# Performance work log

Measured on AMD Instinct MI355X. Metric: run time of the kernel, lower is better.

Reference implementation:

```python
import jax, jax.numpy as jnp
import numpy as np

EPS = 1e-5

def _ln(x, g, b):
    m = jnp.mean(x, axis=-1, keepdims=True)
    v = jnp.mean((x - m) ** 2, axis=-1, keepdims=True)
    return (x - m) * jax.lax.rsqrt(v + EPS) * g + b


def setup_inputs() -> dict:
    key = jax.random.key(0)
    B, T, C, H, A = 4, 1024, 1024, 16, 64
    ks = jax.random.split(key, 16)
    s = 0.02
    inp = {
        "x": jax.random.normal(ks[0], (B, T, C), jnp.float32),
        "ln1_g": jnp.ones((C,), jnp.float32), "ln1_b": jnp.zeros((C,), jnp.float32),
        "ln2_g": jnp.ones((C,), jnp.float32), "ln2_b": jnp.zeros((C,), jnp.float32),
        "ln3_g": jnp.ones((C,), jnp.float32), "ln3_b": jnp.zeros((C,), jnp.float32),
        "wq": jax.random.normal(ks[1], (C, C), jnp.float32) * s, "bq": jnp.zeros((C,), jnp.float32),
        "wk": jax.random.normal(ks[2], (C, C), jnp.float32) * s, "bk": jnp.zeros((C,), jnp.float32),
        "wv": jax.random.normal(ks[3], (C, C), jnp.float32) * s, "bv": jnp.zeros((C,), jnp.float32),
        "wo": jax.random.normal(ks[4], (C, C), jnp.float32) * s, "bo": jnp.zeros((C,), jnp.float32),
        "w1": jax.random.normal(ks[5], (C, 4 * C), jnp.float32) * s, "b1": jnp.zeros((4 * C,), jnp.float32),
        "w2": jax.random.normal(ks[6], (4 * C, C), jnp.float32) * s, "b2": jnp.zeros((C,), jnp.float32),
        "wd": jax.random.normal(ks[7], (C, A), jnp.float32) * 1e-4, "bd": jnp.zeros((A,), jnp.float32),
        "wu": jax.random.normal(ks[8], (A, C), jnp.float32) * 1e-4, "bu": jnp.zeros((C,), jnp.float32),
    }
    return inp


def _block(x, ln1_g, ln1_b, ln2_g, ln2_b, ln3_g, ln3_b,
           wq, bq, wk, bk, wv, bv, wo, bo, w1, b1, w2, b2, wd, bd, wu, bu):
    B, T, C = x.shape
    H = 16
    D = C // H
    normed = _ln(x, ln3_g, ln3_b)  # ln3 of original input, used by adapter

    # --- causal self-attention on ln1(x) ---
    h = _ln(x, ln1_g, ln1_b)
    q = (h @ wq + bq).reshape(B, T, H, D)
    k = (h @ wk + bk).reshape(B, T, H, D)
    v = (h @ wv + bv).reshape(B, T, H, D)
    att = jnp.einsum('bqhd,bkhd->bhqk', q, k) * (1.0 / np.sqrt(D))
    causal = jnp.tril(jnp.ones((T, T), bool))
    att = jnp.where(causal, att, -jnp.inf)
    att = jax.nn.softmax(att, axis=-1)
    y = jnp.einsum('bhqk,bkhd->bqhd', att, v).reshape(B, T, C)
    attn_out = y @ wo + bo

    hidden = x + attn_out
    # --- MLP on ln2(hidden) ---
    m = _ln(hidden, ln2_g, ln2_b)
    mlp_out = jax.nn.gelu(m @ w1 + b1, approximate=False) @ w2 + b2
    forward_states = hidden + mlp_out

    # --- adapter on ln3(original x) ---
    a = jax.nn.relu(normed @ wd + bd) @ wu + bu

    # dropout is identity (p=0 / eval)
    return hidden + forward_states + a


def reference(x, ln1_g, ln1_b, ln2_g, ln2_b, ln3_g, ln3_b,
              wq, bq, wk, bk, wv, bv, wo, bo, w1, b1, w2, b2, wd, bd, wu, bu):
    return _block(x, ln1_g, ln1_b, ln2_g, ln2_b, ln3_g, ln3_b,
                  wq, bq, wk, bk, wv, bv, wo, bo, w1, b1, w2, b2, wd, bd, wu, bu)
```

## Files before the change

### kernel.cpp

```cpp
#include <hip/hip_runtime.h>

typedef unsigned short u16;
typedef __bf16 bf16x8 __attribute__((ext_vector_type(8)));
typedef u16    u16x8  __attribute__((ext_vector_type(8)));
typedef float  f32x4  __attribute__((ext_vector_type(4)));

__device__ __forceinline__ u16 f2bf(float f) {
    union { float f; unsigned u; } x{f};
    unsigned r = x.u + 0x7fffu + ((x.u >> 16) & 1u);
    return (u16)(r >> 16);
}

__device__ __forceinline__ f32x4 mfma16(bf16x8 a, bf16x8 b, f32x4 c) {
    return __builtin_amdgcn_mfma_f32_16x16x32_bf16(a, b, c, 0, 0, 0);
}

__device__ __forceinline__ void async_ld16(const void* g, void* l) {
    __builtin_amdgcn_global_load_lds(
        (const __attribute__((address_space(1))) unsigned int*)g,
        (__attribute__((address_space(3))) unsigned int*)l, 16, 0, 0);
}

__global__ void transpose4_to_bf16(const float* __restrict__ s0, const float* __restrict__ s1,
                                   const float* __restrict__ s2, const float* __restrict__ s3,
                                   u16* __restrict__ d0, u16* __restrict__ d1,
                                   u16* __restrict__ d2, u16* __restrict__ d3) {
    const float* srcs[4] = {s0, s1, s2, s3};
    u16* dsts[4] = {d0, d1, d2, d3};
    const float* __restrict__ in = srcs[blockIdx.z];
    u16* __restrict__ out = dsts[blockIdx.z];
    __shared__ float tile[64][65];
    const int k0 = blockIdx.y * 64, n0 = blockIdx.x * 64;
    const int tid = threadIdx.x;
    const int rr = tid >> 4, cc = tid & 15;
#pragma unroll
    for (int it = 0; it < 4; ++it) {
        const int r = rr + it * 16;
        float4 v = *(const float4*)(in + (long)(k0 + r) * 1024 + n0 + cc * 4);
        tile[r][cc * 4 + 0] = v.x; tile[r][cc * 4 + 1] = v.y;
        tile[r][cc * 4 + 2] = v.z; tile[r][cc * 4 + 3] = v.w;
    }
    __syncthreads();
#pragma unroll
    for (int it = 0; it < 4; ++it) {
        const int n = rr + it * 16;
        ushort4 o;
        o.x = f2bf(tile[cc * 4 + 0][n]);
        o.y = f2bf(tile[cc * 4 + 1][n]);
        o.z = f2bf(tile[cc * 4 + 2][n]);
        o.w = f2bf(tile[cc * 4 + 3][n]);
        *(ushort4*)(out + (long)(n0 + n) * 1024 + k0 + cc * 4) = o;
    }
}

__global__ void transpose_to_bf16(const float* __restrict__ in, u16* __restrict__ out,
                                  int K, int N) {
    __shared__ float tile[64][65];
    const int k0 = blockIdx.y * 64, n0 = blockIdx.x * 64;
    const int tid = threadIdx.x;
    const int rr = tid >> 4, cc = tid & 15;
#pragma unroll
    for (int it = 0; it < 4; ++it) {
        const int r = rr + it * 16;
        float4 v = *(const float4*)(in + (long)(k0 + r) * N + n0 + cc * 4);
        tile[r][cc * 4 + 0] = v.x; tile[r][cc * 4 + 1] = v.y;
        tile[r][cc * 4 + 2] = v.z; tile[r][cc * 4 + 3] = v.w;
    }
    __syncthreads();
#pragma unroll
    for (int it = 0; it < 4; ++it) {
        const int n = rr + it * 16;
        ushort4 o;
        o.x = f2bf(tile[cc * 4 + 0][n]);
        o.y = f2bf(tile[cc * 4 + 1][n]);
        o.z = f2bf(tile[cc * 4 + 2][n]);
        o.w = f2bf(tile[cc * 4 + 3][n]);
        *(ushort4*)(out + (long)(n0 + n) * K + k0 + cc * 4) = o;
    }
}

__global__ void concat_bias(const float* __restrict__ bq, const float* __restrict__ bk,
                            const float* __restrict__ bv, float* __restrict__ out) {
    int i = blockIdx.x * 256 + threadIdx.x;
    out[i] = i < 1024 ? bq[i] : (i < 2048 ? bk[i - 1024] : bv[i - 2048]);
}

__global__ void ln_dual_kernel(const float* __restrict__ x,
                               const float* __restrict__ g1, const float* __restrict__ b1,
                               const float* __restrict__ g3, const float* __restrict__ b3,
                               u16* __restrict__ out1, u16* __restrict__ out3) {
    const int row = blockIdx.x;
    const long base = (long)row * 1024;
    const int t = threadIdx.x;
    float4 v = ((const float4*)(x + base))[t];
    float s = v.x + v.y + v.z + v.w;
    float ss = v.x * v.x + v.y * v.y + v.z * v.z + v.w * v.w;
    for (int o = 32; o > 0; o >>= 1) { s += __shfl_down(s, o); ss += __shfl_down(ss, o); }
    __shared__ float red[8];
    if ((t & 63) == 0) { red[t >> 6] = s; red[(t >> 6) + 4] = ss; }
    __syncthreads();
    float sum = red[0] + red[1] + red[2] + red[3];
    float sq  = red[4] + red[5] + red[6] + red[7];
    const float mean = sum * (1.f / 1024.f);
    const float rstd = rsqrtf(sq * (1.f / 1024.f) - mean * mean + 1e-5f);
    float4 G1 = ((const float4*)g1)[t], B1 = ((const float4*)b1)[t];
    float4 G3 = ((const float4*)g3)[t], B3 = ((const float4*)b3)[t];
    float n0 = (v.x - mean) * rstd, n1 = (v.y - mean) * rstd;
    float n2 = (v.z - mean) * rstd, n3 = (v.w - mean) * rstd;
    ushort4 o1, o3;
    o1.x = f2bf(n0 * G1.x + B1.x); o1.y = f2bf(n1 * G1.y + B1.y);
    o1.z = f2bf(n2 * G1.z + B1.z); o1.w = f2bf(n3 * G1.w + B1.w);
    o3.x = f2bf(n0 * G3.x + B3.x); o3.y = f2bf(n1 * G3.y + B3.y);
    o3.z = f2bf(n2 * G3.z + B3.z); o3.w = f2bf(n3 * G3.w + B3.w);
    ((ushort4*)(out1 + base))[t] = o1;
    ((ushort4*)(out3 + base))[t] = o3;
}

__global__ void ln_single_kernel(const float* __restrict__ x,
                                 const float* __restrict__ g, const float* __restrict__ b,
                                 u16* __restrict__ out) {
    const int row = blockIdx.x;
    const long base = (long)row * 1024;
    const int t = threadIdx.x;
    float4 v = ((const float4*)(x + base))[t];
    float s = v.x + v.y + v.z + v.w;
    float ss = v.x * v.x + v.y * v.y + v.z * v.z + v.w * v.w;
    for (int o = 32; o > 0; o >>= 1) { s += __shfl_down(s, o); ss += __shfl_down(ss, o); }
    __shared__ float red[8];
    if ((t & 63) == 0) { red[t >> 6] = s; red[(t >> 6) + 4] = ss; }
    __syncthreads();
    float sum = red[0] + red[1] + red[2] + red[3];
    float sq  = red[4] + red[5] + red[6] + red[7];
    const float mean = sum * (1.f / 1024.f);
    const float rstd = rsqrtf(sq * (1.f / 1024.f) - mean * mean + 1e-5f);
    float4 G = ((const float4*)g)[t], B = ((const float4*)b)[t];
    ushort4 o;
    o.x = f2bf((v.x - mean) * rstd * G.x + B.x);
    o.y = f2bf((v.y - mean) * rstd * G.y + B.y);
    o.z = f2bf((v.z - mean) * rstd * G.z + B.z);
    o.w = f2bf((v.w - mean) * rstd * G.w + B.w);
    ((ushort4*)(out + base))[t] = o;
}

__global__ void transpose_v(const u16* __restrict__ qkv, u16* __restrict__ vT) {
    const int bh = blockIdx.z, b = bh >> 4, hh = bh & 15;
    const int t0 = blockIdx.x * 32, d0 = blockIdx.y * 32;
    __shared__ u16 tile[32][33];
    const u16* src = qkv + (long)(b * 1024) * 3072 + 2048 + hh * 64;
    for (int i = threadIdx.y; i < 32; i += 8)
        tile[i][threadIdx.x] = src[(long)(t0 + i) * 3072 + d0 + threadIdx.x];
    __syncthreads();
    u16* dst = vT + (long)bh * 64 * 1024;
    for (int i = threadIdx.y; i < 32; i += 8)
        dst[(long)(d0 + i) * 1024 + t0 + threadIdx.x] = tile[threadIdx.x][i];
}

template <int BN, typename Epi>
__global__ __launch_bounds__(256, (BN == 128) ? 3 : 4)
void gemm_kernel(const u16* __restrict__ A, const u16* __restrict__ Bt,
                 int M, int N, int K, int ld, Epi epi) {
    constexpr int AE = 128 * 32;
    constexpr int BE = BN * 32;
    constexpr int MI = (BN == 128) ? 4 : 2;
    __shared__ u16 sm[3][AE + BE];
    const int tid = threadIdx.x;
    const int m0 = blockIdx.y * 128;
    const int n0 = blockIdx.x * BN;
    const int k0g = blockIdx.z * K;
    const int wid = tid >> 6, lane = tid & 63;
    const int lr = lane & 15, lh = lane >> 4;
    const int wm = (BN == 128) ? (wid >> 1) * 64 : wid * 32;
    const int wn = (BN == 128) ? (wid & 1) * 64 : 0;

    const int cr = lane >> 2, lq = lane & 3;
    const int ra0 = wid * 32 + cr, ra1 = ra0 + 16;
    const int qa0 = lq ^ (ra0 & 3) ^ ((ra0 >> 2) & 3);
    const int qa1 = lq ^ (ra1 & 3) ^ ((ra1 >> 2) & 3);
    const long aoff0 = (long)(m0 + ra0) * ld + k0g + qa0 * 8;
    const long aoff1 = (long)(m0 + ra1) * ld + k0g + qa1 * 8;
    const int la0 = wid * 1024, la1 = la0 + 512;

    long boff0, boff1 = 0;
    int lb0, lb1 = 0;
    if (BN == 128) {
        boff0 = (long)min(n0 + ra0, N - 1) * ld + k0g + qa0 * 8;
        boff1 = (long)min(n0 + ra1, N - 1) * ld + k0g + qa1 * 8;
        lb0 = AE + wid * 1024; lb1 = lb0 + 512;
    } else {
        const int rb = wid * 16 + cr;
        const int qb = lq ^ (rb & 3) ^ ((rb >> 2) & 3);
        boff0 = (long)min(n0 + rb, N - 1) * ld + k0g + qb * 8;
        lb0 = AE + wid * 512;
    }

    const int qoff = ((lh ^ (lr & 3) ^ ((lr >> 2) & 3)) & 3) * 8;

    f32x4 acc[MI][4] = {};
    const int nk = K / 32;

    auto stage = [&](int kt) {
        const long ko = (long)kt * 32;
        u16* s = sm[kt % 3];
        async_ld16(A + aoff0 + ko, s + la0);
        async_ld16(A + aoff1 + ko, s + la1);
        async_ld16(Bt + boff0 + ko, s + lb0);
        if constexpr (BN == 128) async_ld16(Bt + boff1 + ko, s + lb1);
    };
    auto compute = [&](int kt) {
        const u16* sA = sm[kt % 3];
        const u16* sB = sA + AE;
        bf16x8 af[MI], bfr[4];
#pragma unroll
        for (int i = 0; i < MI; ++i)
            af[i] = *(const bf16x8*)(sA + (wm + i * 16 + lr) * 32 + qoff);
#pragma unroll
        for (int j = 0; j < 4; ++j)
            bfr[j] = *(const bf16x8*)(sB + (wn + j * 16 + lr) * 32 + qoff);
#pragma unroll
        for (int i = 0; i < MI; ++i)
#pragma unroll
            for (int j = 0; j < 4; ++j)
                acc[i][j] = mfma16(af[i], bfr[j], acc[i][j]);
    };

    stage(0);
    stage(1);
    __syncthreads();
    for (int kt = 0; kt < nk; ++kt) {
        if (kt + 2 < nk) stage(kt + 2);
        compute(kt);
        __syncthreads();
    }

#pragma unroll
    for (int i = 0; i < MI; ++i)
#pragma unroll
        for (int j = 0; j < 4; ++j) {
            const int col = n0 + wn + j * 16 + lr;
            if (col < N) {
#pragma unroll
                for (int r = 0; r < 4; ++r) {
                    const int row = m0 + wm + i * 16 + lh * 4 + r;
                    epi(row, col, acc[i][j][r]);
                }
            }
        }
}

struct EpiBF16Bias {
    u16* out; const float* bias; int ldo;
    __device__ void operator()(int r, int c, float v) const {
        out[(long)r * ldo + c] = f2bf(v + bias[c]);
    }
};
struct EpiResid {
    float* hidden; const float* bias; const float* x;
    __device__ void operator()(int r, int c, float v) const {
        long i = (long)r * 1024 + c; hidden[i] = v + bias[c] + x[i];
    }
};
struct EpiGelu {
    u16* out; const float* bias;
    __device__ void operator()(int r, int c, float v) const {
        float x = v + bias[c];
        float g = 0.5f * x * (1.f + erff(x * 0.70710678118654752f));
        out[(long)r * 4096 + c] = f2bf(g);
    }
};
struct EpiReluBF16 {
    u16* out; const float* bias;
    __device__ void operator()(int r, int c, float v) const {
        out[(long)r * 64 + c] = f2bf(fmaxf(v + bias[c], 0.f));
    }
};
struct EpiAdapter {
    float* out; const float* bias; const float* hidden;
    __device__ void operator()(int r, int c, float v) const {
        long i = (long)r * 1024 + c; out[i] = 2.f * hidden[i] + v + bias[c];
    }
};
struct EpiAtomicOut {
    float* out; const float* bias;
    __device__ void operator()(int r, int c, float v) const {
        if (blockIdx.z == 0) v += bias[c];
        atomicAdd(out + (long)r * 1024 + c, v);
    }
};

__global__ __launch_bounds__(256, 2)
void attn_kernel(const u16* __restrict__ qkv, const u16* __restrict__ vT,
                 u16* __restrict__ y) {
    const int bh = blockIdx.x, b = bh >> 4, hh = bh & 15;
    const int q0 = blockIdx.y * 128;
    const int tid = threadIdx.x, wid = tid >> 6, lane = tid & 63;
    const int lr = lane & 15, lh = lane >> 4;
    const int qw = q0 + wid * 32;

    __shared__ u16 smK[64 * 72];
    __shared__ u16 smV[64 * 72];
    __shared__ u16 smP[4 * 32 * 72];
    u16* pw = smP + wid * (32 * 72);

    const u16* qbase = qkv + (long)(b * 1024) * 3072 + hh * 64;
    const u16* kbase = qbase + 1024;
    const u16* vbase = vT + (long)bh * 64 * 1024;

    bf16x8 a_q[2][2];
#pragma unroll
    for (int mt = 0; mt < 2; ++mt)
#pragma unroll
        for (int ks = 0; ks < 2; ++ks) {
            uint4 t = *(const uint4*)(qbase + (long)(qw + mt * 16 + lr) * 3072 + ks * 32 + lh * 8);
            a_q[mt][ks] = __builtin_bit_cast(bf16x8, t);
        }

    bf16x8 ones;
    { u16x8 t = {0x3F80, 0x3F80, 0x3F80, 0x3F80, 0x3F80, 0x3F80, 0x3F80, 0x3F80};
      ones = __builtin_bit_cast(bf16x8, t); }

    f32x4 o_acc[2][4] = {};
    f32x4 l_acc[2] = {};
    f32x4 m_run[2] = {{-1e30f, -1e30f, -1e30f, -1e30f}, {-1e30f, -1e30f, -1e30f, -1e30f}};

    const int ntiles = q0 / 64 + 2;
    const int ck = tid >> 3, cs = (tid & 7) * 8;
    const int ck2 = (tid + 256) >> 3, cs2 = ((tid + 256) & 7) * 8;
    for (int kt = 0; kt < ntiles; ++kt) {
        const int k0 = kt * 64;
        __syncthreads();
        {
            uint4 kv0 = *(const uint4*)(kbase + (long)(k0 + ck) * 3072 + cs);
            uint4 kv1 = *(const uint4*)(kbase + (long)(k0 + ck2) * 3072 + cs2);
            *(uint4*)(smK + ck * 72 + cs) = kv0;
            *(uint4*)(smK + ck2 * 72 + cs2) = kv1;
            uint4 vv0 = *(const uint4*)(vbase + (long)ck * 1024 + k0 + cs);
            uint4 vv1 = *(const uint4*)(vbase + (long)ck2 * 1024 + k0 + cs2);
            *(uint4*)(smV + ck * 72 + cs) = vv0;
            *(uint4*)(smV + ck2 * 72 + cs2) = vv1;
        }
        __syncthreads();
        if (k0 > qw + 31) continue;

        bf16x8 bK[4][2];
#pragma unroll
        for (int nt = 0; nt < 4; ++nt)
#pragma unroll
            for (int ks = 0; ks < 2; ++ks)
                bK[nt][ks] = *(const bf16x8*)(smK + (nt * 16 + lr) * 72 + ks * 32 + lh * 8);

        f32x4 s[2][4];
#pragma unroll
        for (int mt = 0; mt < 2; ++mt)
#pragma unroll
            for (int nt = 0; nt < 4; ++nt) {
                f32x4 z = {0.f, 0.f, 0.f, 0.f};
                z = mfma16(a_q[mt][0], bK[nt][0], z);
                z = mfma16(a_q[mt][1], bK[nt][1], z);
                s[mt][nt] = z;
            }
#pragma unroll
        for (int mt = 0; mt < 2; ++mt) {
            const int qb = qw + mt * 16 + lh * 4;
#pragma unroll
            for (int nt = 0; nt < 4; ++nt) {
                const int kkg = k0 + nt * 16 + lr;
#pragma unroll
                for (int r = 0; r < 4; ++r) {
                    float v = s[mt][nt][r] * 0.125f;
                    if (kkg > qb + r) v = -1e30f;
                    s[mt][nt][r] = v;
                }
            }
        }
#pragma unroll
        for (int mt = 0; mt < 2; ++mt) {
            f32x4 mx = s[mt][0];
#pragma unroll
            for (int nt = 1; nt < 4; ++nt)
#pragma unroll
                for (int r = 0; r < 4; ++r) mx[r] = fmaxf(mx[r], s[mt][nt][r]);
#pragma unroll
            for (int xm = 1; xm < 16; xm <<= 1)
#pragma unroll
                for (int r = 0; r < 4; ++r) mx[r] = fmaxf(mx[r], __shfl_xor(mx[r], xm));
            f32x4 mnew, alpha;
#pragma unroll
            for (int r = 0; r < 4; ++r) {
                mnew[r] = fmaxf(m_run[mt][r], mx[r]);
                alpha[r] = __expf(m_run[mt][r] - mnew[r]);
            }
            m_run[mt] = mnew;
            l_acc[mt] *= alpha;
#pragma unroll
            for (int dt = 0; dt < 4; ++dt) o_acc[mt][dt] *= alpha;
#pragma unroll
            for (int nt = 0; nt < 4; ++nt)
#pragma unroll
                for (int r = 0; r < 4; ++r)
                    s[mt][nt][r] = __expf(s[mt][nt][r] - mnew[r]);
#pragma unroll
            for (int nt = 0; nt < 4; ++nt)
#pragma unroll
                for (int r = 0; r < 4; ++r)
                    pw[(mt * 16 + lh * 4 + r) * 72 + nt * 16 + lr] = f2bf(s[mt][nt][r]);
        }
        bf16x8 vf[4][2];
#pragma unroll
        for (int dt = 0; dt < 4; ++dt)
#pragma unroll
            for (int ks = 0; ks < 2; ++ks)
                vf[dt][ks] = *(const bf16x8*)(smV + (dt * 16 + lr) * 72 + ks * 32 + lh * 8);
#pragma unroll
        for (int mt = 0; mt < 2; ++mt) {
            bf16x8 pf0 = *(const bf16x8*)(pw + (mt * 16 + lr) * 72 + lh * 8);
            bf16x8 pf1 = *(const bf16x8*)(pw + (mt * 16 + lr) * 72 + 32 + lh * 8);
            l_acc[mt] = mfma16(pf0, ones, l_acc[mt]);
            l_acc[mt] = mfma16(pf1, ones, l_acc[mt]);
#pragma unroll
            for (int dt = 0; dt < 4; ++dt) {
                o_acc[mt][dt] = mfma16(pf0, vf[dt][0], o_acc[mt][dt]);
                o_acc[mt][dt] = mfma16(pf1, vf[dt][1], o_acc[mt][dt]);
            }
        }
    }
#pragma unroll
    for (int mt = 0; mt < 2; ++mt) {
        f32x4 linv;
#pragma unroll
        for (int r = 0; r < 4; ++r) linv[r] = 1.f / l_acc[mt][r];
#pragma unroll
        for (int dt = 0; dt < 4; ++dt) {
#pragma unroll
            for (int r = 0; r < 4; ++r) {
                const int tok = b * 1024 + qw + mt * 16 + lh * 4 + r;
                y[(long)tok * 1024 + hh * 64 + dt * 16 + lr] = f2bf(o_acc[mt][dt][r] * linv[r]);
            }
        }
    }
}

extern "C" void kernel_launch(void* const* d_in, const int* in_sizes, int n_in,
                              void* d_out, int out_size, void* d_ws, size_t ws_size,
                              hipStream_t stream) {
    const float* x    = (const float*)d_in[0];
    const float* ln1g = (const float*)d_in[1];
    const float* ln1b = (const float*)d_in[2];
    const float* ln2g = (const float*)d_in[3];
    const float* ln2b = (const float*)d_in[4];
    const float* ln3g = (const float*)d_in[5];
    const float* ln3b = (const float*)d_in[6];
    const float* wq = (const float*)d_in[7];  const float* bq = (const float*)d_in[8];
    const float* wk = (const float*)d_in[9];  const float* bk = (const float*)d_in[10];
    const float* wv = (const float*)d_in[11]; const float* bv = (const float*)d_in[12];
    const float* wo = (const float*)d_in[13]; const float* bo = (const float*)d_in[14];
    const float* w1 = (const float*)d_in[15]; const float* b1 = (const float*)d_in[16];
    const float* w2 = (const float*)d_in[17]; const float* b2 = (const float*)d_in[18];
    const float* wd = (const float*)d_in[19]; const float* bd = (const float*)d_in[20];
    const float* wu = (const float*)d_in[21]; const float* bu = (const float*)d_in[22];
    float* out = (float*)d_out;

    char* base = (char*)d_ws;
    size_t off = 0;
    auto carve = [&](size_t bytes) -> char* {
        char* p = base + off; off += (bytes + 255) & ~(size_t)255; return p;
    };
    u16* qkv_wt = (u16*)carve(3072L * 1024 * 2);
    u16* wo_t   = (u16*)carve(1024L * 1024 * 2);
    u16* w1_t   = (u16*)carve(4096L * 1024 * 2);
    u16* w2_t   = (u16*)carve(1024L * 4096 * 2);
    u16* wd_t   = (u16*)carve(64L * 1024 * 2);
    u16* wu_t   = (u16*)carve(1024L * 64 * 2);
    float* bqkv = (float*)carve(3072L * 4);
    u16* hbuf   = (u16*)carve(4096L * 1024 * 2);
    u16* nrm    = (u16*)carve(4096L * 1024 * 2);
    u16* qkvb   = (u16*)carve(4096L * 3072 * 2);
    u16* vT     = (u16*)carve(64L * 64 * 1024 * 2);
    u16* ybuf   = (u16*)carve(4096L * 1024 * 2);
    float* hid  = (float*)carve(4096L * 1024 * 4);
    u16* mbuf   = (u16*)carve(4096L * 1024 * 2);
    u16* act    = (u16*)carve(4096L * 4096 * 2);
    u16* t1     = (u16*)carve(4096L * 64 * 2);

    transpose4_to_bf16<<<dim3(16, 16, 4), 256, 0, stream>>>(
        wq, wk, wv, wo, qkv_wt, qkv_wt + 1024L * 1024, qkv_wt + 2048L * 1024, wo_t);
    transpose_to_bf16<<<dim3(64, 16), 256, 0, stream>>>(w1, w1_t, 1024, 4096);
    transpose_to_bf16<<<dim3(16, 64), 256, 0, stream>>>(w2, w2_t, 4096, 1024);
    transpose_to_bf16<<<dim3(1, 16), 256, 0, stream>>>(wd, wd_t, 1024, 64);
    transpose_to_bf16<<<dim3(16, 1), 256, 0, stream>>>(wu, wu_t, 64, 1024);
    concat_bias<<<12, 256, 0, stream>>>(bq, bk, bv, bqkv);

    ln_dual_kernel<<<4096, 256, 0, stream>>>(x, ln1g, ln1b, ln3g, ln3b, hbuf, nrm);

    gemm_kernel<128><<<dim3(24, 32), 256, 0, stream>>>(hbuf, qkv_wt, 4096, 3072, 1024, 1024,
                                                       EpiBF16Bias{qkvb, bqkv, 3072});
    transpose_v<<<dim3(32, 2, 64), dim3(32, 8), 0, stream>>>(qkvb, vT);
    attn_kernel<<<dim3(64, 8), 256, 0, stream>>>(qkvb, vT, ybuf);
    gemm_kernel<64><<<dim3(16, 32), 256, 0, stream>>>(ybuf, wo_t, 4096, 1024, 1024, 1024,
                                                      EpiResid{hid, bo, x});
    ln_single_kernel<<<4096, 256, 0, stream>>>(hid, ln2g, ln2b, mbuf);
    gemm_kernel<128><<<dim3(32, 32), 256, 0, stream>>>(mbuf, w1_t, 4096, 4096, 1024, 1024,
                                                       EpiGelu{act, b1});
    gemm_kernel<64><<<dim3(1, 32), 256, 0, stream>>>(nrm, wd_t, 4096, 64, 1024, 1024,
                                                     EpiReluBF16{t1, bd});
    gemm_kernel<64><<<dim3(16, 32), 256, 0, stream>>>(t1, wu_t, 4096, 1024, 64, 64,
                                                      EpiAdapter{out, bu, hid});
    gemm_kernel<128><<<dim3(8, 32, 2), 256, 0, stream>>>(act, w2_t, 4096, 1024, 2048, 4096,
                                                         EpiAtomicOut{out, b2});
}
```

Measured before the change: 445.0 us.

## Deepen GEMM pipeline to 4 stages and replace split-K atomics with reduction

```diff
diff --git a/kernel.cpp b/kernel.cpp
--- a/kernel.cpp
+++ b/kernel.cpp
@@ -155,14 +155,29 @@
         dst[(long)(d0 + i) * 1024 + t0 + threadIdx.x] = tile[threadIdx.x][i];
 }
 
+__global__ void reduce_out(float* __restrict__ out, const float* __restrict__ p0,
+                           const float* __restrict__ p1, const float* __restrict__ b2) {
+    const long base = (long)blockIdx.x * 1024;
+    const int t = threadIdx.x;
+    float4 a = ((const float4*)(p0 + base))[t];
+    float4 b = ((const float4*)(p1 + base))[t];
+    float4 bias = ((const float4*)b2)[t];
+    float4 o = ((const float4*)(out + base))[t];
+    o.x += a.x + b.x + bias.x;
+    o.y += a.y + b.y + bias.y;
+    o.z += a.z + b.z + bias.z;
+    o.w += a.w + b.w + bias.w;
+    ((float4*)(out + base))[t] = o;
+}
+
 template <int BN, typename Epi>
-__global__ __launch_bounds__(256, (BN == 128) ? 3 : 4)
+__global__ __launch_bounds__(256, (BN == 128) ? 2 : 3)
 void gemm_kernel(const u16* __restrict__ A, const u16* __restrict__ Bt,
                  int M, int N, int K, int ld, Epi epi) {
     constexpr int AE = 128 * 32;
     constexpr int BE = BN * 32;
     constexpr int MI = (BN == 128) ? 4 : 2;
-    __shared__ u16 sm[3][AE + BE];
+    __shared__ u16 sm[4][AE + BE];
     const int tid = threadIdx.x;
     const int m0 = blockIdx.y * 128;
     const int n0 = blockIdx.x * BN;
@@ -200,14 +215,14 @@
 
     auto stage = [&](int kt) {
         const long ko = (long)kt * 32;
-        u16* s = sm[kt % 3];
+        u16* s = sm[kt & 3];
         async_ld16(A + aoff0 + ko, s + la0);
         async_ld16(A + aoff1 + ko, s + la1);
         async_ld16(Bt + boff0 + ko, s + lb0);
         if constexpr (BN == 128) async_ld16(Bt + boff1 + ko, s + lb1);
     };
     auto compute = [&](int kt) {
-        const u16* sA = sm[kt % 3];
+        const u16* sA = sm[kt & 3];
         const u16* sB = sA + AE;
         bf16x8 af[MI], bfr[4];
 #pragma unroll
@@ -226,9 +241,11 @@
     stage(0);
     stage(1);
     __syncthreads();
-    for (int kt = 0; kt < nk; ++kt) {
+    for (int kt = 0; kt < nk; kt += 2) {
         if (kt + 2 < nk) stage(kt + 2);
+        if (kt + 3 < nk) stage(kt + 3);
         compute(kt);
+        compute(kt + 1);
         __syncthreads();
     }
 
@@ -279,11 +296,10 @@
         long i = (long)r * 1024 + c; out[i] = 2.f * hidden[i] + v + bias[c];
     }
 };
-struct EpiAtomicOut {
-    float* out; const float* bias;
+struct EpiStoreSplit {
+    float* p;
     __device__ void operator()(int r, int c, float v) const {
-        if (blockIdx.z == 0) v += bias[c];
-        atomicAdd(out + (long)r * 1024 + c, v);
+        p[(long)blockIdx.z * (4096L * 1024) + (long)r * 1024 + c] = v;
     }
 };
 
@@ -480,6 +496,7 @@
     u16* mbuf   = (u16*)carve(4096L * 1024 * 2);
     u16* act    = (u16*)carve(4096L * 4096 * 2);
     u16* t1     = (u16*)carve(4096L * 64 * 2);
+    float* part = (float*)carve(2L * 4096 * 1024 * 4);
 
     transpose4_to_bf16<<<dim3(16, 16, 4), 256, 0, stream>>>(
         wq, wk, wv, wo, qkv_wt, qkv_wt + 1024L * 1024, qkv_wt + 2048L * 1024, wo_t);
@@ -505,5 +522,6 @@
     gemm_kernel<64><<<dim3(16, 32), 256, 0, stream>>>(t1, wu_t, 4096, 1024, 64, 64,
                                                       EpiAdapter{out, bu, hid});
     gemm_kernel<128><<<dim3(8, 32, 2), 256, 0, stream>>>(act, w2_t, 4096, 1024, 2048, 4096,
-                                                         EpiAtomicOut{out, b2});
-}
+                                                         EpiStoreSplit{part});
+    reduce_out<<<4096, 256, 0, stream>>>(out, part, part + 4096L * 1024, b2);
+}
```

Measured after the change: 413.9 us. 7.0% less time.

## Use double buffering for higher occupancy and split-K=4 with bf16 partials plus reduction

Applied to the files above, without the earlier changes.

```diff
diff --git a/kernel.cpp b/kernel.cpp
--- a/kernel.cpp
+++ b/kernel.cpp
@@ -9,6 +9,10 @@
     union { float f; unsigned u; } x{f};
     unsigned r = x.u + 0x7fffu + ((x.u >> 16) & 1u);
     return (u16)(r >> 16);
+}
+__device__ __forceinline__ float bf2f(u16 h) {
+    union { unsigned u; float f; } x{(unsigned)h << 16};
+    return x.f;
 }
 
 __device__ __forceinline__ f32x4 mfma16(bf16x8 a, bf16x8 b, f32x4 c) {
@@ -155,14 +159,32 @@
         dst[(long)(d0 + i) * 1024 + t0 + threadIdx.x] = tile[threadIdx.x][i];
 }
 
+__global__ void reduce_out4(float* __restrict__ out, const u16* __restrict__ p,
+                            const float* __restrict__ b2) {
+    const long base = (long)blockIdx.x * 1024;
+    const int t = threadIdx.x;
+    float4 sum = {0.f, 0.f, 0.f, 0.f};
+#pragma unroll
+    for (int z = 0; z < 4; ++z) {
+        ushort4 q = ((const ushort4*)(p + (long)z * (4096L * 1024) + base))[t];
+        sum.x += bf2f(q.x); sum.y += bf2f(q.y);
+        sum.z += bf2f(q.z); sum.w += bf2f(q.w);
+    }
+    float4 bias = ((const float4*)b2)[t];
+    float4 o = ((const float4*)(out + base))[t];
+    o.x += sum.x + bias.x; o.y += sum.y + bias.y;
+    o.z += sum.z + bias.z; o.w += sum.w + bias.w;
+    ((float4*)(out + base))[t] = o;
+}
+
 template <int BN, typename Epi>
-__global__ __launch_bounds__(256, (BN == 128) ? 3 : 4)
+__global__ __launch_bounds__(256, 4)
 void gemm_kernel(const u16* __restrict__ A, const u16* __restrict__ Bt,
                  int M, int N, int K, int ld, Epi epi) {
     constexpr int AE = 128 * 32;
     constexpr int BE = BN * 32;
     constexpr int MI = (BN == 128) ? 4 : 2;
-    __shared__ u16 sm[3][AE + BE];
+    __shared__ u16 sm[2][AE + BE];
     const int tid = threadIdx.x;
     const int m0 = blockIdx.y * 128;
     const int n0 = blockIdx.x * BN;
@@ -200,14 +222,14 @@
 
     auto stage = [&](int kt) {
         const long ko = (long)kt * 32;
-        u16* s = sm[kt % 3];
+        u16* s = sm[kt & 1];
         async_ld16(A + aoff0 + ko, s + la0);
         async_ld16(A + aoff1 + ko, s + la1);
         async_ld16(Bt + boff0 + ko, s + lb0);
         if constexpr (BN == 128) async_ld16(Bt + boff1 + ko, s + lb1);
     };
     auto compute = [&](int kt) {
-        const u16* sA = sm[kt % 3];
+        const u16* sA = sm[kt & 1];
         const u16* sB = sA + AE;
         bf16x8 af[MI], bfr[4];
 #pragma unroll
@@ -224,10 +246,9 @@
     };
 
     stage(0);
-    stage(1);
     __syncthreads();
     for (int kt = 0; kt < nk; ++kt) {
-        if (kt + 2 < nk) stage(kt + 2);
+        if (kt + 1 < nk) stage(kt + 1);
         compute(kt);
         __syncthreads();
     }
@@ -279,11 +300,10 @@
         long i = (long)r * 1024 + c; out[i] = 2.f * hidden[i] + v + bias[c];
     }
 };
-struct EpiAtomicOut {
-    float* out; const float* bias;
+struct EpiStoreSplit {
+    u16* p;
     __device__ void operator()(int r, int c, float v) const {
-        if (blockIdx.z == 0) v += bias[c];
-        atomicAdd(out + (long)r * 1024 + c, v);
+        p[(long)blockIdx.z * (4096L * 1024) + (long)r * 1024 + c] = f2bf(v);
     }
 };
 
@@ -480,6 +500,7 @@
     u16* mbuf   = (u16*)carve(4096L * 1024 * 2);
     u16* act    = (u16*)carve(4096L * 4096 * 2);
     u16* t1     = (u16*)carve(4096L * 64 * 2);
+    u16* part   = (u16*)carve(4L * 4096 * 1024 * 2);
 
     transpose4_to_bf16<<<dim3(16, 16, 4), 256, 0, stream>>>(
         wq, wk, wv, wo, qkv_wt, qkv_wt + 1024L * 1024, qkv_wt + 2048L * 1024, wo_t);
@@ -504,6 +525,7 @@
                                                      EpiReluBF16{t1, bd});
     gemm_kernel<64><<<dim3(16, 32), 256, 0, stream>>>(t1, wu_t, 4096, 1024, 64, 64,
                                                       EpiAdapter{out, bu, hid});
-    gemm_kernel<128><<<dim3(8, 32, 2), 256, 0, stream>>>(act, w2_t, 4096, 1024, 2048, 4096,
-                                                         EpiAtomicOut{out, b2});
-}
+    gemm_kernel<128><<<dim3(8, 32, 4), 256, 0, stream>>>(act, w2_t, 4096, 1024, 1024, 4096,
+                                                         EpiStoreSplit{part});
+    reduce_out4<<<4096, 256, 0, stream>>>(out, part, b2);
+}
```

After: 424.1 us. 4.7% less time.
